# Kernel optimization log

Measured on AMD Instinct MI355X. Metric: run time of the kernel, lower is better.

The kernel has to match this reference:

```python
import jax, jax.numpy as jnp
import numpy as np

# Model dims (match init_kwargs)
B, S, IN = 8, 96, 128          # batch, seq_len, control+data bits
H, M, N = 2, 32, 512           # heads, memory content size, memory addresses
STATE, OUT, NS = 256, 126, 3   # hidden state, output (data bits), shift size
EPS = 1e-12
# per-head interface parameter layout: s, jd, j, gamma, erase, add, k, beta, g
_SPLITS = [NS, 1, 3, 1, M, M, M, 1, 1]
_OFFS = np.concatenate([[0], np.cumsum(_SPLITS)])


def setup_inputs() -> dict:
    key = jax.random.key(0)
    ks = jax.random.split(key, 4)
    CIN = IN + H * M + STATE  # controller input: x ++ read ++ state
    return {
        "x": jax.random.normal(ks[0], (B, S, IN), jnp.float32),
        "W_s": jax.random.normal(ks[1], (CIN, STATE), jnp.float32) * 0.05,
        "b_s": jnp.zeros((STATE,), jnp.float32),
        "W_o": jax.random.normal(ks[2], (CIN, OUT), jnp.float32) * 0.05,
        "b_o": jnp.zeros((OUT,), jnp.float32),
        "W_u": jax.random.normal(ks[3], (CIN, int(_OFFS[-1]) * H), jnp.float32) * 0.05,
        "b_u": jnp.zeros((int(_OFFS[-1]) * H,), jnp.float32),
    }


def _circular_conv(wt, s):
    # wt: [B,H,N], s: [B,H,NS] softmax shift kernel centered at 0
    out = jnp.zeros_like(wt)
    c = NS // 2
    for i in range(NS):
        out = out + s[..., i:i + 1] * jnp.roll(wt, shift=i - c, axis=-1)
    return out


def _dwm_forward(x, W_s, b_s, W_o, b_o, W_u, b_u):
    b = x.shape[0]
    state0 = jnp.ones((b, STATE), x.dtype)
    wt0 = jnp.zeros((b, H, N), x.dtype).at[:, :, 0].set(1.0)
    mem0 = jnp.full((b, M, N), 0.01, x.dtype)

    def step(carry, x_t):
        state, wt, wt_dyn, mem = carry
        # ---- read: attention over memory addresses ----
        read = jnp.einsum('bhn,bmn->bhm', wt, mem).reshape(b, H * M)
        comb = jnp.concatenate([x_t, read, state], axis=-1)
        # ---- controller ----
        state_n = jax.nn.sigmoid(comb @ W_s + b_s)
        out_t = comb @ W_o + b_o
        upd = (comb @ W_u + b_u).reshape(b, H, int(_OFFS[-1]))
        sp = [upd[..., int(_OFFS[i]):int(_OFFS[i + 1])] for i in range(len(_SPLITS))]
        s, jd, j, gamma, erase, add, k, beta, g = sp
        s = jax.nn.softmax(jax.nn.softplus(s), axis=-1)
        jd = jax.nn.sigmoid(jd)
        j = jax.nn.softmax(j, axis=-1)
        gamma = 1.0 + jax.nn.softplus(gamma)
        erase = jax.nn.sigmoid(erase)
        k = jnp.tanh(k)
        beta = jax.nn.softplus(beta)
        g = jax.nn.sigmoid(g)
        # ---- memory write (erase then add, NTM-style multi-head) ----
        mem = mem * jnp.prod(1.0 - erase[:, :, :, None] * wt[:, :, None, :], axis=1)
        mem = mem + jnp.einsum('bhm,bhn->bmn', add, wt)
        # ---- content addressing (cosine similarity) ----
        k_n = k / (jnp.linalg.norm(k, axis=-1, keepdims=True) + EPS)
        m_n = mem / (jnp.linalg.norm(mem, axis=1, keepdims=True) + EPS)
        wt_k = jnp.einsum('bhm,bmn->bhn', k_n, m_n)
        wt_c = g * jax.nn.softmax(beta * wt_k, axis=-1) + (1.0 - g) * wt
        # ---- shift + sharpen + renormalize ----
        wt_sh = (_circular_conv(wt_c, s) + EPS) ** gamma
        wt_n = wt_sh / jnp.sum(wt_sh, axis=-1, keepdims=True)
        # ---- bookmark (snapshot) update + jump interpolation ----
        wt_a0 = jnp.zeros_like(wt_n).at[..., 0].set(1.0)
        wt_dyn_n = (1.0 - jd) * wt_dyn + jd * wt_n
        wt_f = j[..., 0:1] * wt_n + j[..., 1:2] * wt_a0 + j[..., 2:3] * wt_dyn
        return (state_n, wt_f, wt_dyn_n, mem), out_t

    _, outs = jax.lax.scan(step, (state0, wt0, wt0, mem0), jnp.swapaxes(x, 0, 1))
    return jnp.swapaxes(outs, 0, 1)  # [B, S, OUT]


def reference(x, W_s, b_s, W_o, b_o, W_u, b_u):
    return _dwm_forward(x, W_s, b_s, W_o, b_o, W_u, b_u)
```

## Files before the change

kernel.cpp:

```cpp
#include <hip/hip_runtime.h>
#include <math.h>

#define NTHREADS 1024

namespace {
constexpr int kB = 8, kS = 96, kIN = 128, kH = 2, kM = 32, kN = 512;
constexpr int kSTATE = 256, kOUT = 126, kUH = 106;
constexpr int kNC = 594;
constexpr int kKR = 320;
constexpr int kMLD = 520;
constexpr float kEPS = 1e-12f;
constexpr int kXWfloats = kB * kS * kNC;
constexpr size_t kWbOffBytes = (size_t)kXWfloats * 4;
}

__device__ __forceinline__ float sigm_(float x) { return 1.0f / (1.0f + __expf(-x)); }
__device__ __forceinline__ float splus_(float x) { return x > 20.0f ? x : __logf(1.0f + __expf(x)); }

__global__ __launch_bounds__(640) void prep_xw(
    const float* __restrict__ x,
    const float* __restrict__ Ws, const float* __restrict__ bs,
    const float* __restrict__ Wo, const float* __restrict__ bo,
    const float* __restrict__ Wu, const float* __restrict__ bu,
    float* __restrict__ xw)
{
    __shared__ float sx[kIN];
    const int row = blockIdx.x;
    const int t = threadIdx.x;
    if (t < kIN) sx[t] = x[row * kIN + t];
    __syncthreads();
    if (t < kNC) {
        const float* Wp; int ld, j; float acc;
        if (t < 256)      { Wp = Ws; ld = kSTATE;   j = t;       acc = bs[j]; }
        else if (t < 382) { Wp = Wo; ld = kOUT;     j = t - 256; acc = bo[j]; }
        else              { Wp = Wu; ld = kH * kUH; j = t - 382; acc = bu[j]; }
        const float* p = Wp + j;
        #pragma unroll 8
        for (int i = 0; i < kIN; ++i) acc = fmaf(sx[i], p[i * ld], acc);
        xw[row * kNC + t] = acc;
    }
}

__global__ __launch_bounds__(1024) void prep_pack(
    const float* __restrict__ Ws, const float* __restrict__ Wo,
    const float* __restrict__ Wu, unsigned short* __restrict__ Wb)
{
    int idx = blockIdx.x * 1024 + threadIdx.x;
    if (idx >= kKR * kNC) return;
    int i = idx / kNC, c = idx - i * kNC;
    float v;
    if (c < 256)      v = Ws[(kIN + i) * kSTATE + c];
    else if (c < 382) v = Wo[(kIN + i) * kOUT + (c - 256)];
    else              v = Wu[(kIN + i) * (kH * kUH) + (c - 382)];
    unsigned int bits = __float_as_uint(v);
    unsigned int r = (bits + 0x7fffu + ((bits >> 16) & 1u)) >> 16;
    Wb[idx] = (unsigned short)r;
}

__global__ __launch_bounds__(NTHREADS) void dwm_kernel(
    const float* __restrict__ xw,
    const unsigned int* __restrict__ Wb,
    float* __restrict__ out)
{
    __shared__ float s_mem[kM * kMLD];
    __shared__ float s_wt[kH * kN];
    __shared__ float s_wtd[kH * kN];
    __shared__ float s_tmp[kH * kN];
    __shared__ float s_comb[kKR];
    __shared__ float s_upd[kH * kUH];
    __shared__ float s_er[kH * kM], s_ad[kH * kM], s_kk[kH * kM];
    __shared__ float s_red[16];
    __shared__ float s_shift[kH][3], s_jmp[kH][3];
    __shared__ float s_jd[kH], s_gam[kH], s_beta[kH], s_g[kH], s_ikn[kH];

    const int b = blockIdx.x;
    const int t = threadIdx.x;
    const int wid = t >> 6;
    const int lane = t & 63;

    for (int i = t; i < kM * kN; i += NTHREADS)
        s_mem[(i >> 9) * kMLD + (i & 511)] = 0.01f;
    for (int i = t; i < kH * kN; i += NTHREADS) {
        float v = ((i & 511) == 0) ? 1.0f : 0.0f;
        s_wt[i] = v; s_wtd[i] = v;
    }
    if (t < kSTATE) s_comb[64 + t] = 1.0f;
    __syncthreads();

    for (int step = 0; step < kS; ++step) {
        {
            int g = t >> 4, l16 = t & 15, h = g >> 5, m = g & 31;
            const float4* w4 = (const float4*)&s_wt[h * kN];
            const float4* m4 = (const float4*)&s_mem[m * kMLD];
            float ax = 0.0f, ay = 0.0f, az = 0.0f, aw = 0.0f;
            #pragma unroll
            for (int k = 0; k < 8; ++k) {
                float4 w = w4[l16 + 16 * k];
                float4 mv = m4[l16 + 16 * k];
                ax = fmaf(w.x, mv.x, ax); ay = fmaf(w.y, mv.y, ay);
                az = fmaf(w.z, mv.z, az); aw = fmaf(w.w, mv.w, aw);
            }
            float acc = (ax + ay) + (az + aw);
            acc += __shfl_xor(acc, 1);
            acc += __shfl_xor(acc, 2);
            acc += __shfl_xor(acc, 4);
            acc += __shfl_xor(acc, 8);
            if (l16 == 0) s_comb[g] = acc;
        }
        __syncthreads();

        float a0 = 0.0f, a1 = 0.0f;
        if (t < 297) {
            const unsigned int* wp = Wb + t;
            const float* xr = &xw[(b * kS + step) * kNC + 2 * t];
            a0 = xr[0]; a1 = xr[1];
            #pragma unroll 8
            for (int i = 0; i < kKR; ++i) {
                unsigned int u = wp[i * 297];
                float c = s_comb[i];
                a0 = fmaf(__uint_as_float(u << 16), c, a0);
                a1 = fmaf(__uint_as_float(u & 0xffff0000u), c, a1);
            }
        }
        __syncthreads();

        if (t < 297) {
            int c0 = 2 * t;
            if (c0 < kSTATE) {
                s_comb[64 + c0] = sigm_(a0);
                s_comb[65 + c0] = sigm_(a1);
            } else if (c0 < kSTATE + kOUT) {
                float* o = &out[(b * kS + step) * kOUT];
                o[c0 - 256] = a0; o[c0 - 255] = a1;
            } else {
                int i0 = c0 - 382;
                auto disp = [&](int idx, float v) {
                    int h = idx >= kUH;
                    int j = idx - (h ? kUH : 0);
                    if (j >= 8 && j < 40)        s_er[h * kM + j - 8]  = sigm_(v);
                    else if (j >= 40 && j < 72)  s_ad[h * kM + j - 40] = v;
                    else if (j >= 72 && j < 104) s_kk[h * kM + j - 72] = tanhf(v);
                    else s_upd[idx] = v;
                };
                disp(i0, a0);
                disp(i0 + 1, a1);
            }
        }
        __syncthreads();

        if (t < 64) {
            int h = t >> 5, m = t & 31;
            float kv = s_kk[t];
            float ss = kv * kv;
            ss += __shfl_xor(ss, 1);
            ss += __shfl_xor(ss, 2);
            ss += __shfl_xor(ss, 4);
            ss += __shfl_xor(ss, 8);
            ss += __shfl_xor(ss, 16);
            if (m == 0) s_ikn[h] = 1.0f / (sqrtf(ss) + kEPS);
        } else if (t == 64 || t == 65) {
            int h = t - 64;
            const float* u = &s_upd[h * kUH];
            float b0 = splus_(u[0]), b1 = splus_(u[1]), b2 = splus_(u[2]);
            float mx = fmaxf(b0, fmaxf(b1, b2));
            float e0 = __expf(b0 - mx), e1 = __expf(b1 - mx), e2 = __expf(b2 - mx);
            float inv = 1.0f / (e0 + e1 + e2);
            s_shift[h][0] = e0 * inv; s_shift[h][1] = e1 * inv; s_shift[h][2] = e2 * inv;
            s_jd[h] = sigm_(u[3]);
            b0 = u[4]; b1 = u[5]; b2 = u[6];
            mx = fmaxf(b0, fmaxf(b1, b2));
            e0 = __expf(b0 - mx); e1 = __expf(b1 - mx); e2 = __expf(b2 - mx);
            inv = 1.0f / (e0 + e1 + e2);
            s_jmp[h][0] = e0 * inv; s_jmp[h][1] = e1 * inv; s_jmp[h][2] = e2 * inv;
            s_gam[h]  = 1.0f + splus_(u[7]);
            s_beta[h] = splus_(u[104]);
            s_g[h]    = sigm_(u[105]);
        }
        {
            int tn = t & 127, tm = t >> 7;
            int n0 = tn << 2;
            float4 w0v = *(const float4*)&s_wt[n0];
            float4 w1v = *(const float4*)&s_wt[kN + n0];
            #pragma unroll
            for (int r = 0; r < 4; ++r) {
                int m = tm + (r << 3);
                float er0 = s_er[m], er1 = s_er[kM + m];
                float ad0 = s_ad[m], ad1 = s_ad[kM + m];
                float4* mp = (float4*)&s_mem[m * kMLD + n0];
                float4 v = *mp;
                v.x = v.x * (1.0f - er0 * w0v.x) * (1.0f - er1 * w1v.x) + ad0 * w0v.x + ad1 * w1v.x;
                v.y = v.y * (1.0f - er0 * w0v.y) * (1.0f - er1 * w1v.y) + ad0 * w0v.y + ad1 * w1v.y;
                v.z = v.z * (1.0f - er0 * w0v.z) * (1.0f - er1 * w1v.z) + ad0 * w0v.z + ad1 * w1v.z;
                v.w = v.w * (1.0f - er0 * w0v.w) * (1.0f - er1 * w1v.w) + ad0 * w0v.w + ad1 * w1v.w;
                *mp = v;
            }
        }
        __syncthreads();

        if (t < kN) {
            int n = t;
            float c0 = 0.0f, c1 = 0.0f, ss = 0.0f;
            #pragma unroll
            for (int m = 0; m < kM; ++m) {
                float v = s_mem[m * kMLD + n];
                c0 = fmaf(s_kk[m], v, c0);
                c1 = fmaf(s_kk[kM + m], v, c1);
                ss = fmaf(v, v, ss);
            }
            float invc = 1.0f / (sqrtf(ss) + kEPS);
            s_tmp[n]      = s_beta[0] * (c0 * s_ikn[0] * invc);
            s_tmp[kN + n] = s_beta[1] * (c1 * s_ikn[1] * invc);
        }
        __syncthreads();

        {
            int h = t >> 9;
            float e = __expf(s_tmp[t]);
            float sm = e;
            sm += __shfl_xor(sm, 1);
            sm += __shfl_xor(sm, 2);
            sm += __shfl_xor(sm, 4);
            sm += __shfl_xor(sm, 8);
            sm += __shfl_xor(sm, 16);
            sm += __shfl_xor(sm, 32);
            if (lane == 0) s_red[wid] = sm;
            __syncthreads();
            float tot = 0.0f;
            #pragma unroll
            for (int i = 0; i < 8; ++i) tot += s_red[h * 8 + i];
            float wc = s_g[h] * e / tot + (1.0f - s_g[h]) * s_wt[t];
            s_tmp[t] = wc;
        }
        __syncthreads();

        {
            int h = t >> 9, n = t & 511;
            const float* wcp = &s_tmp[h * kN];
            float cv = s_shift[h][0] * wcp[(n + 1) & 511]
                     + s_shift[h][1] * wcp[n]
                     + s_shift[h][2] * wcp[(n + 511) & 511];
            float wsh = exp2f(s_gam[h] * __log2f(cv + kEPS));
            float sm = wsh;
            sm += __shfl_xor(sm, 1);
            sm += __shfl_xor(sm, 2);
            sm += __shfl_xor(sm, 4);
            sm += __shfl_xor(sm, 8);
            sm += __shfl_xor(sm, 16);
            sm += __shfl_xor(sm, 32);
            if (lane == 0) s_red[wid] = sm;
            __syncthreads();
            float tot = 0.0f;
            #pragma unroll
            for (int i = 0; i < 8; ++i) tot += s_red[h * 8 + i];
            float wn = wsh / tot;
            float dold = s_wtd[t];
            s_wtd[t] = (1.0f - s_jd[h]) * dold + s_jd[h] * wn;
            float wa0 = (n == 0) ? 1.0f : 0.0f;
            s_wt[t] = s_jmp[h][0] * wn + s_jmp[h][1] * wa0 + s_jmp[h][2] * dold;
        }
        __syncthreads();
    }
}

extern "C" void kernel_launch(void* const* d_in, const int* in_sizes, int n_in,
                              void* d_out, int out_size, void* d_ws, size_t ws_size,
                              hipStream_t stream) {
    const float* x   = (const float*)d_in[0];
    const float* Ws  = (const float*)d_in[1];
    const float* bs  = (const float*)d_in[2];
    const float* Wo  = (const float*)d_in[3];
    const float* bo  = (const float*)d_in[4];
    const float* Wu  = (const float*)d_in[5];
    const float* bu  = (const float*)d_in[6];
    float* outp = (float*)d_out;

    float* xw = (float*)d_ws;
    unsigned short* Wb = (unsigned short*)((char*)d_ws + kWbOffBytes);

    prep_xw<<<dim3(kB * kS), dim3(640), 0, stream>>>(x, Ws, bs, Wo, bo, Wu, bu, xw);
    prep_pack<<<dim3((kKR * kNC + 1023) / 1024), dim3(1024), 0, stream>>>(Ws, Wo, Wu, Wb);
    dwm_kernel<<<dim3(kB), dim3(NTHREADS), 0, stream>>>(xw, (const unsigned int*)Wb, outp);
}
```

Baseline: 1.095 ms.

## Pack bf16 weights along K and keep first 64 row-pairs in registers

Repacks the recurrent controller weights so each 32-bit word holds two consecutive K rows for one output column. Each of 594 threads now computes one output column instead of 297 threads computing two. The first 64 packed rows are preloaded into registers once per block and reused across all 96 steps, which cuts per-step global or L2 weight traffic. The cost is 64 extra VGPRs per thread at 1024 threads per block, which risks register spills. The two-wide comb read becomes a float2 LDS load.

Measured after the change: 2.030 ms. 85.3% more time.

```diff
diff --git a/kernel.cpp b/kernel.cpp
--- a/kernel.cpp
+++ b/kernel.cpp
@@ -8,6 +8,8 @@
 constexpr int kSTATE = 256, kOUT = 126, kUH = 106;
 constexpr int kNC = 594;
 constexpr int kKR = 320;
+constexpr int kRP = 160;
+constexpr int kREG = 64;
 constexpr int kMLD = 520;
 constexpr float kEPS = 1e-12f;
 constexpr int kXWfloats = kB * kS * kNC;
@@ -16,6 +18,8 @@
 
 __device__ __forceinline__ float sigm_(float x) { return 1.0f / (1.0f + __expf(-x)); }
 __device__ __forceinline__ float splus_(float x) { return x > 20.0f ? x : __logf(1.0f + __expf(x)); }
+__device__ __forceinline__ float blo_(unsigned int u) { return __uint_as_float(u << 16); }
+__device__ __forceinline__ float bhi_(unsigned int u) { return __uint_as_float(u & 0xffff0000u); }
 
 __global__ __launch_bounds__(640) void prep_xw(
     const float* __restrict__ x,
@@ -41,20 +45,27 @@
     }
 }
 
+__device__ __forceinline__ unsigned short rtn_bf16_(float v) {
+    unsigned int bits = __float_as_uint(v);
+    return (unsigned short)((bits + 0x7fffu + ((bits >> 16) & 1u)) >> 16);
+}
+
 __global__ __launch_bounds__(1024) void prep_pack(
     const float* __restrict__ Ws, const float* __restrict__ Wo,
-    const float* __restrict__ Wu, unsigned short* __restrict__ Wb)
+    const float* __restrict__ Wu, unsigned int* __restrict__ Wb)
 {
     int idx = blockIdx.x * 1024 + threadIdx.x;
-    if (idx >= kKR * kNC) return;
-    int i = idx / kNC, c = idx - i * kNC;
-    float v;
-    if (c < 256)      v = Ws[(kIN + i) * kSTATE + c];
-    else if (c < 382) v = Wo[(kIN + i) * kOUT + (c - 256)];
-    else              v = Wu[(kIN + i) * (kH * kUH) + (c - 382)];
-    unsigned int bits = __float_as_uint(v);
-    unsigned int r = (bits + 0x7fffu + ((bits >> 16) & 1u)) >> 16;
-    Wb[idx] = (unsigned short)r;
+    if (idx >= kRP * kNC) return;
+    int r = idx / kNC, c = idx - r * kNC;
+    auto fetch = [&](int i) -> float {
+        int row = kIN + i;
+        if (c < 256)      return Ws[row * kSTATE + c];
+        else if (c < 382) return Wo[row * kOUT + (c - 256)];
+        else              return Wu[row * (kH * kUH) + (c - 382)];
+    };
+    unsigned int lo = rtn_bf16_(fetch(2 * r));
+    unsigned int hi = rtn_bf16_(fetch(2 * r + 1));
+    Wb[idx] = (hi << 16) | lo;
 }
 
 __global__ __launch_bounds__(NTHREADS) void dwm_kernel(
@@ -78,6 +89,13 @@
     const int wid = t >> 6;
     const int lane = t & 63;
 
+    unsigned int wr[kREG];
+    const unsigned int* wp = Wb + t;
+    if (t < kNC) {
+        #pragma unroll
+        for (int r = 0; r < kREG; ++r) wr[r] = wp[r * kNC];
+    }
+
     for (int i = t; i < kM * kN; i += NTHREADS)
         s_mem[(i >> 9) * kMLD + (i & 511)] = 0.01f;
     for (int i = t; i < kH * kN; i += NTHREADS) {
@@ -109,41 +127,38 @@
         }
         __syncthreads();
 
-        float a0 = 0.0f, a1 = 0.0f;
-        if (t < 297) {
-            const unsigned int* wp = Wb + t;
-            const float* xr = &xw[(b * kS + step) * kNC + 2 * t];
-            a0 = xr[0]; a1 = xr[1];
-            #pragma unroll 8
-            for (int i = 0; i < kKR; ++i) {
-                unsigned int u = wp[i * 297];
-                float c = s_comb[i];
-                a0 = fmaf(__uint_as_float(u << 16), c, a0);
-                a1 = fmaf(__uint_as_float(u & 0xffff0000u), c, a1);
-            }
-        }
-        __syncthreads();
-
-        if (t < 297) {
-            int c0 = 2 * t;
-            if (c0 < kSTATE) {
-                s_comb[64 + c0] = sigm_(a0);
-                s_comb[65 + c0] = sigm_(a1);
-            } else if (c0 < kSTATE + kOUT) {
-                float* o = &out[(b * kS + step) * kOUT];
-                o[c0 - 256] = a0; o[c0 - 255] = a1;
+        float acc = 0.0f;
+        if (t < kNC) {
+            acc = xw[(b * kS + step) * kNC + t];
+            #pragma unroll
+            for (int r = 0; r < kREG; ++r) {
+                float2 cc = *(const float2*)&s_comb[2 * r];
+                acc = fmaf(blo_(wr[r]), cc.x, acc);
+                acc = fmaf(bhi_(wr[r]), cc.y, acc);
+            }
+            #pragma unroll 16
+            for (int r = kREG; r < kRP; ++r) {
+                unsigned int u = wp[r * kNC];
+                float2 cc = *(const float2*)&s_comb[2 * r];
+                acc = fmaf(blo_(u), cc.x, acc);
+                acc = fmaf(bhi_(u), cc.y, acc);
+            }
+        }
+        __syncthreads();
+
+        if (t < kNC) {
+            if (t < kSTATE) {
+                s_comb[64 + t] = sigm_(acc);
+            } else if (t < kSTATE + kOUT) {
+                out[(b * kS + step) * kOUT + (t - kSTATE)] = acc;
             } else {
-                int i0 = c0 - 382;
-                auto disp = [&](int idx, float v) {
-                    int h = idx >= kUH;
-                    int j = idx - (h ? kUH : 0);
-                    if (j >= 8 && j < 40)        s_er[h * kM + j - 8]  = sigm_(v);
-                    else if (j >= 40 && j < 72)  s_ad[h * kM + j - 40] = v;
-                    else if (j >= 72 && j < 104) s_kk[h * kM + j - 72] = tanhf(v);
-                    else s_upd[idx] = v;
-                };
-                disp(i0, a0);
-                disp(i0 + 1, a1);
+                int idx = t - 382;
+                int h = idx >= kUH;
+                int j = idx - (h ? kUH : 0);
+                if (j >= 8 && j < 40)        s_er[h * kM + j - 8]  = sigm_(acc);
+                else if (j >= 40 && j < 72)  s_ad[h * kM + j - 40] = acc;
+                else if (j >= 72 && j < 104) s_kk[h * kM + j - 72] = tanhf(acc);
+                else s_upd[idx] = acc;
             }
         }
         __syncthreads();
@@ -275,9 +290,9 @@
     float* outp = (float*)d_out;
 
     float* xw = (float*)d_ws;
-    unsigned short* Wb = (unsigned short*)((char*)d_ws + kWbOffBytes);
+    unsigned int* Wb = (unsigned int*)((char*)d_ws + kWbOffBytes);
 
     prep_xw<<<dim3(kB * kS), dim3(640), 0, stream>>>(x, Ws, bs, Wo, bo, Wu, bu, xw);
-    prep_pack<<<dim3((kKR * kNC + 1023) / 1024), dim3(1024), 0, stream>>>(Ws, Wo, Wu, Wb);
-    dwm_kernel<<<dim3(kB), dim3(NTHREADS), 0, stream>>>(xw, (const unsigned int*)Wb, outp);
-}
+    prep_pack<<<dim3((kRP * kNC + 1023) / 1024), dim3(1024), 0, stream>>>(Ws, Wo, Wu, Wb);
+    dwm_kernel<<<dim3(kB), dim3(NTHREADS), 0, stream>>>(xw, Wb, outp);
+}
```
